# Optimization experiments

Hardware: AMD Instinct MI355X
Metric: run time of the kernel (lower is better)

The kernel has to match this reference:

```python
import jax, jax.numpy as jnp
import numpy as np

N_NODES = 100000
N_EDGES = 1600000
D = 128


def setup_inputs() -> dict:
    key = jax.random.key(0)
    k0, k1, k2, k3 = jax.random.split(key, 4)
    x = jax.random.normal(k0, (N_NODES, D), dtype=jnp.float32)
    edge_index = jax.random.randint(k1, (2, N_EDGES), 0, N_NODES, dtype=jnp.int32)
    # Glorot-ish init for GCNConv weights; zero bias (PyG default)
    W1 = jax.random.normal(k2, (D, D), dtype=jnp.float32) / np.sqrt(D).astype(np.float32)
    b1 = jnp.zeros((D,), dtype=jnp.float32)
    W2 = jax.random.normal(k3, (D, D), dtype=jnp.float32) / np.sqrt(D).astype(np.float32)
    b2 = jnp.zeros((D,), dtype=jnp.float32)
    return {"x": x, "edge_index": edge_index, "W1": W1, "b1": b1, "W2": W2, "b2": b2}


def _gcn_layer(x, src, dst, norm, W, b, n_nodes):
    # PyG GCNConv: linear transform first, then normalized aggregation over A+I.
    h = x @ W                                    # [N, D_out]
    coef = norm[src] * norm[dst]                 # [E] symmetric normalization
    msgs = h[src] * coef[:, None]                # [E, D_out] gathered edge messages
    agg = jax.ops.segment_sum(msgs, dst, num_segments=n_nodes)
    agg = agg + h * (norm * norm)[:, None]       # self-loop contribution deg^{-1} * h
    return agg + b


def reference(x, edge_index, W1, b1, W2, b2):
    n_nodes = x.shape[0]
    src, dst = edge_index[0], edge_index[1]
    # degree of A + I (self-loops added), computed on destination nodes
    deg = jax.ops.segment_sum(jnp.ones(src.shape[0], dtype=x.dtype), dst,
                              num_segments=n_nodes) + 1.0
    norm = jax.lax.rsqrt(deg)                    # deg^{-1/2}
    # Layer 1: GCNConv -> ReLU (dropout is identity in eval mode)
    h = jax.nn.relu(_gcn_layer(x, src, dst, norm, W1, b1, n_nodes))
    # Layer 2
    h = jax.nn.relu(_gcn_layer(h, src, dst, norm, W2, b2, n_nodes))
    return h
```

## Files before the change

### kernel.cpp

```cpp
#include <hip/hip_runtime.h>

#define D 128
#define EG 4096
#define PADW 16

typedef _Float16 h8 __attribute__((ext_vector_type(8)));
typedef _Float16 h2 __attribute__((ext_vector_type(2)));
typedef float f4 __attribute__((ext_vector_type(4)));
typedef unsigned u4 __attribute__((ext_vector_type(4)));


__global__ __launch_bounds__(256) void hist_k(const int* __restrict__ dst,
                                              int* __restrict__ counts,
                                              int E, int NB, int G) {
  __shared__ int hist[512];
  int g = blockIdx.x, t = threadIdx.x;
  for (int b = t; b < NB; b += 256) hist[b] = 0;
  __syncthreads();
  int e0 = g * EG;
#pragma unroll
  for (int it = 0; it < EG / 256; ++it) {
    int e = e0 + it * 256 + t;
    if (e < E) atomicAdd(&hist[dst[e] >> 8], 1);
  }
  __syncthreads();
  for (int b = t; b < NB; b += 256) counts[b * G + g] = hist[b];
}

__global__ __launch_bounds__(256) void bsum_k(const int* __restrict__ in,
                                              int* __restrict__ bsum, int M) {
  __shared__ int s[256];
  int t = threadIdx.x, i = blockIdx.x * 256 + t;
  s[t] = (i < M) ? in[i] : 0;
  __syncthreads();
  for (int off = 128; off > 0; off >>= 1) {
    if (t < off) s[t] += s[t + off];
    __syncthreads();
  }
  if (t == 0) bsum[blockIdx.x] = s[0];
}

__global__ __launch_bounds__(1024) void bscan_k(int* bsum, int nb) {
  __shared__ int s[1024];
  int t = threadIdx.x;
  s[t] = (t < nb) ? bsum[t] : 0;
  __syncthreads();
  for (int off = 1; off < 1024; off <<= 1) {
    int v = (t >= off) ? s[t - off] : 0;
    __syncthreads();
    s[t] += v;
    __syncthreads();
  }
  if (t < nb) bsum[t] = s[t];
}

__global__ __launch_bounds__(256) void scanfin_k(const int* __restrict__ in,
                                                 const int* __restrict__ bsum_incl,
                                                 int* __restrict__ outx, int M) {
  __shared__ int s[256];
  int b = blockIdx.x, t = threadIdx.x, i = b * 256 + t;
  int v0 = (i < M) ? in[i] : 0;
  s[t] = v0;
  __syncthreads();
  for (int off = 1; off < 256; off <<= 1) {
    int v = (t >= off) ? s[t - off] : 0;
    __syncthreads();
    s[t] += v;
    __syncthreads();
  }
  int base = (b > 0) ? bsum_incl[b - 1] : 0;
  if (i < M) outx[i] = base + s[t] - v0;
}

__global__ __launch_bounds__(256) void scatter_k(const int* __restrict__ src,
                                                 const int* __restrict__ dst,
                                                 const int* __restrict__ cscan,
                                                 unsigned* __restrict__ tmp,
                                                 int E, int NB, int G) {
  __shared__ int hist[512];
  __shared__ int base[512];
  int g = blockIdx.x, t = threadIdx.x;
  for (int b = t; b < NB; b += 256) {
    hist[b] = 0;
    base[b] = cscan[b * G + g];
  }
  __syncthreads();
  int e0 = g * EG;
#pragma unroll
  for (int it = 0; it < EG / 256; ++it) {
    int e = e0 + it * 256 + t;
    if (e < E) {
      int d = dst[e];
      int b = d >> 8;
      int r = atomicAdd(&hist[b], 1);
      tmp[base[b] + r] = ((unsigned)(d & 255) << 20) | (unsigned)src[e];
    }
  }
}

__global__ __launch_bounds__(256) void bucket_k(const unsigned* __restrict__ tmp,
                                                const int* __restrict__ cscan,
                                                float* __restrict__ nrm,
                                                int2* __restrict__ rs2,
                                                int* __restrict__ eoff,
                                                int N, int E, int NB, int G) {
  __shared__ int cnt[256];
  __shared__ int sc[256];
  __shared__ int cur[256];
  int b = blockIdx.x, t = threadIdx.x;
  int seg0 = cscan[b * G];
  int seg1 = (b == NB - 1) ? E : cscan[(b + 1) * G];
  int pbase = (seg0 + b * (256 * (PADW - 1) + 16) + 15) & ~15;
  cnt[t] = 0;
  __syncthreads();
  for (int i = seg0 + t; i < seg1; i += 256)
    atomicAdd(&cnt[tmp[i] >> 20], 1);
  __syncthreads();
  int v0 = cnt[t];
  int pd = (v0 + PADW - 1) & ~(PADW - 1);
  sc[t] = pd;
  __syncthreads();
  for (int off = 1; off < 256; off <<= 1) {
    int v = (t >= off) ? sc[t - off] : 0;
    __syncthreads();
    sc[t] += v;
    __syncthreads();
  }
  int ex = sc[t] - pd;
  cur[t] = pbase + ex;
  int node = b * 256 + t;
  if (node < N) {
    rs2[node] = make_int2(pbase + ex, pbase + ex + pd);
    nrm[node] = rsqrtf((float)v0 + 1.0f);
  }
  int dummy = N * 256;
  for (int k = v0; k < pd; ++k) eoff[pbase + ex + k] = dummy;
  __syncthreads();
  for (int i = seg0 + t; i < seg1; i += 256) {
    unsigned p = tmp[i];
    int r = atomicAdd(&cur[p >> 20], 1);
    eoff[r] = (int)((p & 0xFFFFF) << 8);
  }
}

__global__ void zero_k(_Float16* __restrict__ Hh, int N) {
  int t = threadIdx.x;
  if (t < 128) Hh[(size_t)N * D + t] = (_Float16)0.f;
}

__global__ __launch_bounds__(256) void wtrans_k(const float* __restrict__ W,
                                                _Float16* __restrict__ WT) {
  int idx = blockIdx.x * 256 + threadIdx.x;
  int k = idx >> 7, col = idx & 127;
  WT[col * D + k] = (_Float16)W[idx];
}

template <bool FP32IN>
__global__ __launch_bounds__(256) void gemm_k(const void* __restrict__ Xv,
                                              const _Float16* __restrict__ WT,
                                              const float* __restrict__ nrm,
                                              _Float16* __restrict__ Hh, int N) {
  __shared__ _Float16 Wl[D * 136];
  int tid = threadIdx.x;
#pragma unroll
  for (int it = 0; it < 8; ++it) {
    int idx = it * 256 + tid;
    int col = idx >> 4, kseg = idx & 15;
    *(h8*)&Wl[col * 136 + kseg * 8] = *(const h8*)&WT[col * D + kseg * 8];
  }
  __syncthreads();
  int wave = tid >> 6, lane = tid & 63;
  int lr = lane & 15, lk = lane >> 4;
#pragma unroll
  for (int tt = 0; tt < 2; ++tt) {
    int tile = blockIdx.x * 8 + wave * 2 + tt;
    int row0 = tile * 16;
    if (row0 >= N) break;
    int row = row0 + lr;
    int rowc = row < N ? row : N - 1;
    h8 a[4];
    if constexpr (FP32IN) {
      const float* X = (const float*)Xv;
#pragma unroll
      for (int ks = 0; ks < 4; ++ks) {
        f4 p = *(const f4*)&X[(size_t)rowc * D + ks * 32 + lk * 8];
        f4 q = *(const f4*)&X[(size_t)rowc * D + ks * 32 + lk * 8 + 4];
        h8 t;
        t[0] = (_Float16)p[0]; t[1] = (_Float16)p[1];
        t[2] = (_Float16)p[2]; t[3] = (_Float16)p[3];
        t[4] = (_Float16)q[0]; t[5] = (_Float16)q[1];
        t[6] = (_Float16)q[2]; t[7] = (_Float16)q[3];
        a[ks] = t;
      }
    } else {
      const _Float16* X = (const _Float16*)Xv;
#pragma unroll
      for (int ks = 0; ks < 4; ++ks)
        a[ks] = *(const h8*)&X[(size_t)rowc * D + ks * 32 + lk * 8];
    }
    f4 acc[8];
#pragma unroll
    for (int ct = 0; ct < 8; ++ct) acc[ct] = (f4){0.f, 0.f, 0.f, 0.f};
#pragma unroll
    for (int ct = 0; ct < 8; ++ct) {
#pragma unroll
      for (int ks = 0; ks < 4; ++ks) {
        h8 b = *(const h8*)&Wl[(ct * 16 + lr) * 136 + ks * 32 + lk * 8];
        acc[ct] = __builtin_amdgcn_mfma_f32_16x16x32_f16(a[ks], b, acc[ct], 0, 0, 0);
      }
    }
#pragma unroll
    for (int r = 0; r < 4; ++r) {
      int ro = row0 + lk * 4 + r;
      if (ro < N) {
        float sc = nrm[ro];
#pragma unroll
        for (int ct = 0; ct < 8; ++ct)
          Hh[(size_t)ro * D + ct * 16 + lr] = (_Float16)(acc[ct][r] * sc);
      }
    }
  }
}

template <bool F16OUT>
__global__ __launch_bounds__(256) void agg_k(const _Float16* __restrict__ Hh,
                                             const float* __restrict__ nrm,
                                             const int2* __restrict__ rs2,
                                             const int* __restrict__ eoff,
                                             const float* __restrict__ bias,
                                             void* __restrict__ outv, int N) {
  int wave = threadIdx.x >> 6, lane = threadIdx.x & 63;
  int n = blockIdx.x * 4 + wave;
  if (n >= N) return;
  int grp = lane >> 4, sub = lane & 15;
  unsigned soff = (unsigned)sub * 16u;
  int2 se = rs2[n];
  const char* base = (const char*)Hh;
  const h2 ones = {(_Float16)1.f, (_Float16)1.f};
  float acc[8] = {};
  int i = se.x;
  if (i < se.y) {
    u4 offs = *(const u4*)&eoff[i + grp * 4];
    while (true) {
      u4 v0 = *(const u4*)(base + offs[0] + soff);
      u4 v1 = *(const u4*)(base + offs[1] + soff);
      u4 v2 = *(const u4*)(base + offs[2] + soff);
      u4 v3 = *(const u4*)(base + offs[3] + soff);
      i += PADW;
      bool more = i < se.y;
      u4 offn;
      if (more) offn = *(const u4*)&eoff[i + grp * 4];
#pragma unroll
      for (int k = 0; k < 4; ++k) {
        unsigned lo01 = __builtin_amdgcn_perm(v1[k], v0[k], 0x05040100u);
        unsigned hi01 = __builtin_amdgcn_perm(v1[k], v0[k], 0x07060302u);
        unsigned lo23 = __builtin_amdgcn_perm(v3[k], v2[k], 0x05040100u);
        unsigned hi23 = __builtin_amdgcn_perm(v3[k], v2[k], 0x07060302u);
        acc[2 * k] = __builtin_amdgcn_fdot2(__builtin_bit_cast(h2, lo01), ones,
                                            acc[2 * k], false);
        acc[2 * k + 1] = __builtin_amdgcn_fdot2(__builtin_bit_cast(h2, hi01), ones,
                                                acc[2 * k + 1], false);
        acc[2 * k] = __builtin_amdgcn_fdot2(__builtin_bit_cast(h2, lo23), ones,
                                            acc[2 * k], false);
        acc[2 * k + 1] = __builtin_amdgcn_fdot2(__builtin_bit_cast(h2, hi23), ones,
                                                acc[2 * k + 1], false);
      }
      if (!more) break;
      offs = offn;
    }
  }
#pragma unroll
  for (int j = 0; j < 8; ++j) acc[j] += __shfl_xor(acc[j], 16);
#pragma unroll
  for (int j = 0; j < 8; ++j) acc[j] += __shfl_xor(acc[j], 32);
  if (grp == 0) {
    int d0 = sub * 8;
    h8 hv = *(const h8*)&Hh[(size_t)n * D + d0];
    float nn = nrm[n];
    f4 bl = *(const f4*)&bias[d0];
    f4 bh = *(const f4*)&bias[d0 + 4];
    float o[8];
#pragma unroll
    for (int j = 0; j < 8; ++j) {
      float bj = (j < 4) ? bl[j] : bh[j - 4];
      o[j] = fmaxf((acc[j] + (float)hv[j]) * nn + bj, 0.f);
    }
    if constexpr (F16OUT) {
      _Float16* out = (_Float16*)outv;
      h8 ov;
#pragma unroll
      for (int j = 0; j < 8; ++j) ov[j] = (_Float16)o[j];
      *(h8*)&out[(size_t)n * D + d0] = ov;
    } else {
      float* out = (float*)outv;
      f4 lo = {o[0], o[1], o[2], o[3]};
      f4 hi = {o[4], o[5], o[6], o[7]};
      *(f4*)&out[(size_t)n * D + d0] = lo;
      *(f4*)&out[(size_t)n * D + d0 + 4] = hi;
    }
  }
}


extern "C" void kernel_launch(void* const* d_in, const int* in_sizes, int n_in,
                              void* d_out, int out_size, void* d_ws, size_t ws_size,
                              hipStream_t stream) {
  const float* x  = (const float*)d_in[0];
  const int*   ei = (const int*)d_in[1];
  const float* W1 = (const float*)d_in[2];
  const float* b1 = (const float*)d_in[3];
  const float* W2 = (const float*)d_in[4];
  const float* b2 = (const float*)d_in[5];
  float* out = (float*)d_out;

  int N = in_sizes[0] / D;
  int E = in_sizes[1] / 2;
  const int* srcp = ei;
  const int* dstp = ei + E;

  int NB = (N + 255) / 256;
  int G  = (E + EG - 1) / EG;
  int M  = NB * G;
  int nbM = (M + 255) / 256;

  char* ws = (char*)d_ws;
  size_t off = 0;
  auto alloc = [&](size_t bytes) -> char* {
    char* p = ws + off;
    off = (off + bytes + 511) & ~(size_t)511;
    return p;
  };
  _Float16* Hh   = (_Float16*)alloc((size_t)(N + 1) * D * 2);
  _Float16* O1h  = (_Float16*)alloc((size_t)N * D * 2);
  float* normv     = (float*)alloc((size_t)N * 4);
  int2*  rs2       = (int2*)alloc((size_t)N * 8);
  int*   counts    = (int*)alloc((size_t)M * 4);
  int*   cscan     = (int*)alloc((size_t)M * 4);
  unsigned* tmp    = (unsigned*)alloc((size_t)E * 4);
  int*   eoff      = (int*)alloc((size_t)(E + (size_t)NB * (256 * (PADW - 1) + 16) + 16) * 4);
  int*   bsum      = (int*)alloc(4096);
  _Float16* WT1    = (_Float16*)alloc((size_t)D * D * 2);
  _Float16* WT2    = (_Float16*)alloc((size_t)D * D * 2);

  int tiles = (N + 15) / 16;
  int nbGemm = (tiles + 7) / 8;
  int nbAgg = (N + 3) / 4;

  wtrans_k<<<64, 256, 0, stream>>>(W1, WT1);
  wtrans_k<<<64, 256, 0, stream>>>(W2, WT2);
  zero_k<<<1, 128, 0, stream>>>(Hh, N);

  hist_k<<<G, 256, 0, stream>>>(dstp, counts, E, NB, G);
  bsum_k<<<nbM, 256, 0, stream>>>(counts, bsum, M);
  bscan_k<<<1, 1024, 0, stream>>>(bsum, nbM);
  scanfin_k<<<nbM, 256, 0, stream>>>(counts, bsum, cscan, M);
  scatter_k<<<G, 256, 0, stream>>>(srcp, dstp, cscan, tmp, E, NB, G);
  bucket_k<<<NB, 256, 0, stream>>>(tmp, cscan, normv, rs2, eoff, N, E, NB, G);

  gemm_k<true><<<nbGemm, 256, 0, stream>>>(x, WT1, normv, Hh, N);
  agg_k<true><<<nbAgg, 256, 0, stream>>>(Hh, normv, rs2, eoff, b1, O1h, N);
  gemm_k<false><<<nbGemm, 256, 0, stream>>>(O1h, WT2, normv, Hh, N);
  agg_k<false><<<nbAgg, 256, 0, stream>>>(Hh, normv, rs2, eoff, b2, out, N);
}
```

Before: 215.7 us.

## Fold self-loop into CSR, merge prep and scan kernels, use nontemporal accesses

Each node's self-loop is now written as an explicit first edge in its padded CSR segment, so the aggregation no longer reads its own row separately in the epilogue. The padding slot size changes to match, and every node now has at least one edge. The tiny weight-transpose and zero kernels become one prep kernel, and the single-block scan is folded into the final scan, with each block summing its preceding block totals. Aggregation uses nontemporal loads for edge offsets and nontemporal stores for outputs. Together these cut launch count and some memory traffic, at the cost of a redundant partial-sum loop per scan block and one extra gather per node.

```diff
diff --git a/kernel.cpp b/kernel.cpp
--- a/kernel.cpp
+++ b/kernel.cpp
@@ -40,25 +40,24 @@
   if (t == 0) bsum[blockIdx.x] = s[0];
 }
 
-__global__ __launch_bounds__(1024) void bscan_k(int* bsum, int nb) {
-  __shared__ int s[1024];
-  int t = threadIdx.x;
-  s[t] = (t < nb) ? bsum[t] : 0;
-  __syncthreads();
-  for (int off = 1; off < 1024; off <<= 1) {
-    int v = (t >= off) ? s[t - off] : 0;
-    __syncthreads();
-    s[t] += v;
-    __syncthreads();
-  }
-  if (t < nb) bsum[t] = s[t];
-}
-
-__global__ __launch_bounds__(256) void scanfin_k(const int* __restrict__ in,
-                                                 const int* __restrict__ bsum_incl,
-                                                 int* __restrict__ outx, int M) {
+__global__ __launch_bounds__(256) void scanfin2_k(const int* __restrict__ in,
+                                                  const int* __restrict__ bsum,
+                                                  int* __restrict__ outx, int M) {
   __shared__ int s[256];
+  __shared__ int bsh;
   int b = blockIdx.x, t = threadIdx.x, i = b * 256 + t;
+  int part = 0;
+  for (int k = t; k < b; k += 256) part += bsum[k];
+  s[t] = part;
+  __syncthreads();
+  for (int off = 128; off > 0; off >>= 1) {
+    if (t < off) s[t] += s[t + off];
+    __syncthreads();
+  }
+  if (t == 0) bsh = s[0];
+  __syncthreads();
+  int base = bsh;
+  __syncthreads();
   int v0 = (i < M) ? in[i] : 0;
   s[t] = v0;
   __syncthreads();
@@ -68,7 +67,6 @@
     s[t] += v;
     __syncthreads();
   }
-  int base = (b > 0) ? bsum_incl[b - 1] : 0;
   if (i < M) outx[i] = base + s[t] - v0;
 }
 
@@ -110,14 +108,15 @@
   int b = blockIdx.x, t = threadIdx.x;
   int seg0 = cscan[b * G];
   int seg1 = (b == NB - 1) ? E : cscan[(b + 1) * G];
-  int pbase = (seg0 + b * (256 * (PADW - 1) + 16) + 15) & ~15;
+  int pbase = (seg0 + b * 4112 + 15) & ~15;
   cnt[t] = 0;
   __syncthreads();
   for (int i = seg0 + t; i < seg1; i += 256)
     atomicAdd(&cnt[tmp[i] >> 20], 1);
   __syncthreads();
+  int node = b * 256 + t;
   int v0 = cnt[t];
-  int pd = (v0 + PADW - 1) & ~(PADW - 1);
+  int pd = (node < N) ? ((v0 + 1 + PADW - 1) & ~(PADW - 1)) : 0;
   sc[t] = pd;
   __syncthreads();
   for (int off = 1; off < 256; off <<= 1) {
@@ -127,14 +126,15 @@
     __syncthreads();
   }
   int ex = sc[t] - pd;
-  cur[t] = pbase + ex;
-  int node = b * 256 + t;
+  int rbeg = pbase + ex;
+  cur[t] = rbeg + 1;
   if (node < N) {
-    rs2[node] = make_int2(pbase + ex, pbase + ex + pd);
+    rs2[node] = make_int2(rbeg, rbeg + pd);
     nrm[node] = rsqrtf((float)v0 + 1.0f);
-  }
-  int dummy = N * 256;
-  for (int k = v0; k < pd; ++k) eoff[pbase + ex + k] = dummy;
+    eoff[rbeg] = node * 256;
+    int dummy = N * 256;
+    for (int k = v0 + 1; k < pd; ++k) eoff[rbeg + k] = dummy;
+  }
   __syncthreads();
   for (int i = seg0 + t; i < seg1; i += 256) {
     unsigned p = tmp[i];
@@ -143,16 +143,21 @@
   }
 }
 
-__global__ void zero_k(_Float16* __restrict__ Hh, int N) {
-  int t = threadIdx.x;
-  if (t < 128) Hh[(size_t)N * D + t] = (_Float16)0.f;
-}
-
-__global__ __launch_bounds__(256) void wtrans_k(const float* __restrict__ W,
-                                                _Float16* __restrict__ WT) {
-  int idx = blockIdx.x * 256 + threadIdx.x;
-  int k = idx >> 7, col = idx & 127;
-  WT[col * D + k] = (_Float16)W[idx];
+__global__ __launch_bounds__(256) void prep_k(const float* __restrict__ W1,
+                                              const float* __restrict__ W2,
+                                              _Float16* __restrict__ WT1,
+                                              _Float16* __restrict__ WT2,
+                                              _Float16* __restrict__ Hh, int N) {
+  int b = blockIdx.x, t = threadIdx.x;
+  if (b < 128) {
+    const float* W = (b < 64) ? W1 : W2;
+    _Float16* WT = (b < 64) ? WT1 : WT2;
+    int idx = (b & 63) * 256 + t;
+    int k = idx >> 7, col = idx & 127;
+    WT[col * D + k] = (_Float16)W[idx];
+  } else if (t < 128) {
+    Hh[(size_t)N * D + t] = (_Float16)0.f;
+  }
 }
 
 template <bool FP32IN>
@@ -239,35 +244,33 @@
   const h2 ones = {(_Float16)1.f, (_Float16)1.f};
   float acc[8] = {};
   int i = se.x;
-  if (i < se.y) {
-    u4 offs = *(const u4*)&eoff[i + grp * 4];
-    while (true) {
-      u4 v0 = *(const u4*)(base + offs[0] + soff);
-      u4 v1 = *(const u4*)(base + offs[1] + soff);
-      u4 v2 = *(const u4*)(base + offs[2] + soff);
-      u4 v3 = *(const u4*)(base + offs[3] + soff);
-      i += PADW;
-      bool more = i < se.y;
-      u4 offn;
-      if (more) offn = *(const u4*)&eoff[i + grp * 4];
-#pragma unroll
-      for (int k = 0; k < 4; ++k) {
-        unsigned lo01 = __builtin_amdgcn_perm(v1[k], v0[k], 0x05040100u);
-        unsigned hi01 = __builtin_amdgcn_perm(v1[k], v0[k], 0x07060302u);
-        unsigned lo23 = __builtin_amdgcn_perm(v3[k], v2[k], 0x05040100u);
-        unsigned hi23 = __builtin_amdgcn_perm(v3[k], v2[k], 0x07060302u);
-        acc[2 * k] = __builtin_amdgcn_fdot2(__builtin_bit_cast(h2, lo01), ones,
-                                            acc[2 * k], false);
-        acc[2 * k + 1] = __builtin_amdgcn_fdot2(__builtin_bit_cast(h2, hi01), ones,
-                                                acc[2 * k + 1], false);
-        acc[2 * k] = __builtin_amdgcn_fdot2(__builtin_bit_cast(h2, lo23), ones,
-                                            acc[2 * k], false);
-        acc[2 * k + 1] = __builtin_amdgcn_fdot2(__builtin_bit_cast(h2, hi23), ones,
-                                                acc[2 * k + 1], false);
-      }
-      if (!more) break;
-      offs = offn;
-    }
+  u4 offs = __builtin_nontemporal_load((const u4*)&eoff[i + grp * 4]);
+  while (true) {
+    u4 v0 = *(const u4*)(base + offs[0] + soff);
+    u4 v1 = *(const u4*)(base + offs[1] + soff);
+    u4 v2 = *(const u4*)(base + offs[2] + soff);
+    u4 v3 = *(const u4*)(base + offs[3] + soff);
+    i += PADW;
+    bool more = i < se.y;
+    u4 offn;
+    if (more) offn = __builtin_nontemporal_load((const u4*)&eoff[i + grp * 4]);
+#pragma unroll
+    for (int k = 0; k < 4; ++k) {
+      unsigned lo01 = __builtin_amdgcn_perm(v1[k], v0[k], 0x05040100u);
+      unsigned hi01 = __builtin_amdgcn_perm(v1[k], v0[k], 0x07060302u);
+      unsigned lo23 = __builtin_amdgcn_perm(v3[k], v2[k], 0x05040100u);
+      unsigned hi23 = __builtin_amdgcn_perm(v3[k], v2[k], 0x07060302u);
+      acc[2 * k] = __builtin_amdgcn_fdot2(__builtin_bit_cast(h2, lo01), ones,
+                                          acc[2 * k], false);
+      acc[2 * k + 1] = __builtin_amdgcn_fdot2(__builtin_bit_cast(h2, hi01), ones,
+                                              acc[2 * k + 1], false);
+      acc[2 * k] = __builtin_amdgcn_fdot2(__builtin_bit_cast(h2, lo23), ones,
+                                          acc[2 * k], false);
+      acc[2 * k + 1] = __builtin_amdgcn_fdot2(__builtin_bit_cast(h2, hi23), ones,
+                                              acc[2 * k + 1], false);
+    }
+    if (!more) break;
+    offs = offn;
   }
 #pragma unroll
   for (int j = 0; j < 8; ++j) acc[j] += __shfl_xor(acc[j], 16);
@@ -275,7 +278,6 @@
   for (int j = 0; j < 8; ++j) acc[j] += __shfl_xor(acc[j], 32);
   if (grp == 0) {
     int d0 = sub * 8;
-    h8 hv = *(const h8*)&Hh[(size_t)n * D + d0];
     float nn = nrm[n];
     f4 bl = *(const f4*)&bias[d0];
     f4 bh = *(const f4*)&bias[d0 + 4];
@@ -283,20 +285,20 @@
 #pragma unroll
     for (int j = 0; j < 8; ++j) {
       float bj = (j < 4) ? bl[j] : bh[j - 4];
-      o[j] = fmaxf((acc[j] + (float)hv[j]) * nn + bj, 0.f);
+      o[j] = fmaxf(acc[j] * nn + bj, 0.f);
     }
     if constexpr (F16OUT) {
       _Float16* out = (_Float16*)outv;
       h8 ov;
 #pragma unroll
       for (int j = 0; j < 8; ++j) ov[j] = (_Float16)o[j];
-      *(h8*)&out[(size_t)n * D + d0] = ov;
+      __builtin_nontemporal_store(ov, (h8*)&out[(size_t)n * D + d0]);
     } else {
       float* out = (float*)outv;
       f4 lo = {o[0], o[1], o[2], o[3]};
       f4 hi = {o[4], o[5], o[6], o[7]};
-      *(f4*)&out[(size_t)n * D + d0] = lo;
-      *(f4*)&out[(size_t)n * D + d0 + 4] = hi;
+      __builtin_nontemporal_store(lo, (f4*)&out[(size_t)n * D + d0]);
+      __builtin_nontemporal_store(hi, (f4*)&out[(size_t)n * D + d0 + 4]);
     }
   }
 }
@@ -337,7 +339,7 @@
   int*   counts    = (int*)alloc((size_t)M * 4);
   int*   cscan     = (int*)alloc((size_t)M * 4);
   unsigned* tmp    = (unsigned*)alloc((size_t)E * 4);
-  int*   eoff      = (int*)alloc((size_t)(E + (size_t)NB * (256 * (PADW - 1) + 16) + 16) * 4);
+  int*   eoff      = (int*)alloc((size_t)(E + (size_t)NB * 4112 + 64) * 4);
   int*   bsum      = (int*)alloc(4096);
   _Float16* WT1    = (_Float16*)alloc((size_t)D * D * 2);
   _Float16* WT2    = (_Float16*)alloc((size_t)D * D * 2);
@@ -346,14 +348,11 @@
   int nbGemm = (tiles + 7) / 8;
   int nbAgg = (N + 3) / 4;
 
-  wtrans_k<<<64, 256, 0, stream>>>(W1, WT1);
-  wtrans_k<<<64, 256, 0, stream>>>(W2, WT2);
-  zero_k<<<1, 128, 0, stream>>>(Hh, N);
+  prep_k<<<129, 256, 0, stream>>>(W1, W2, WT1, WT2, Hh, N);
 
   hist_k<<<G, 256, 0, stream>>>(dstp, counts, E, NB, G);
   bsum_k<<<nbM, 256, 0, stream>>>(counts, bsum, M);
-  bscan_k<<<1, 1024, 0, stream>>>(bsum, nbM);
-  scanfin_k<<<nbM, 256, 0, stream>>>(counts, bsum, cscan, M);
+  scanfin2_k<<<nbM, 256, 0, stream>>>(counts, bsum, cscan, M);
   scatter_k<<<G, 256, 0, stream>>>(srcp, dstp, cscan, tmp, E, NB, G);
   bucket_k<<<NB, 256, 0, stream>>>(tmp, cscan, normv, rs2, eoff, N, E, NB, G);
 
```

New measurement: 215.8 us. Within noise of the previous version (+0.0%).
